# Optimization experiments

Measured on AMD Instinct MI355X. Metric: run time of the kernel, lower is better.

The kernel has to match this reference:

```python
import jax, jax.numpy as jnp
import numpy as np
import math

D_MODEL = 96
D_STATE = 16
D_CONV = 3
EXPAND = 2
D_INNER = EXPAND * D_MODEL          # 192
DT_RANK = math.ceil(D_MODEL / 16)   # 6
B_SZ, H_SZ, W_SZ = 2, 56, 56


def setup_inputs() -> dict:
    key = jax.random.key(0)
    ks = jax.random.split(key, 10)
    x = jax.random.normal(ks[0], (B_SZ, H_SZ, W_SZ, D_MODEL), jnp.float32)
    W_in = jax.random.normal(ks[1], (D_MODEL, 2 * D_INNER), jnp.float32) * 0.02
    conv_w = jax.random.normal(ks[2], (D_CONV, D_CONV, 1, D_INNER), jnp.float32) * 0.1
    conv_b = jax.random.normal(ks[3], (D_INNER,), jnp.float32) * 0.02
    W_xproj = jax.random.normal(ks[4], (D_INNER, DT_RANK + 2 * D_STATE), jnp.float32) * 0.02
    dt_std = DT_RANK ** -0.5
    W_dt = jax.random.uniform(ks[5], (DT_RANK, D_INNER), jnp.float32, -dt_std, dt_std)
    # dt_proj bias init: inverse-softplus of dt ~ LogUniform(dt_min, dt_max)
    dt_min, dt_max = 1e-3, 1e-1
    dt = jnp.exp(jax.random.uniform(ks[6], (D_INNER,), jnp.float32)
                 * (math.log(dt_max) - math.log(dt_min)) + math.log(dt_min))
    dt = jnp.clip(dt, 1e-4, None)
    b_dt = dt + jnp.log(-jnp.expm1(-dt))
    # A_log initialized to broadcast arange(1..d_state) (as in the source, no log taken)
    A_log = jnp.tile(jnp.arange(1, D_STATE + 1, dtype=jnp.float32)[None, :], (D_INNER, 1))
    D_skip = jnp.ones((D_INNER,), jnp.float32)
    W_out = jax.random.normal(ks[7], (D_INNER, D_MODEL), jnp.float32) * 0.02
    return {"x": x, "W_in": W_in, "conv_w": conv_w, "conv_b": conv_b,
            "W_xproj": W_xproj, "W_dt": W_dt, "b_dt": b_dt,
            "A_log": A_log, "D_skip": D_skip, "W_out": W_out}


def _selective_scan(xs, dt, A, Bm, Cm, D_skip):
    """Canonical Mamba selective scan.
    xs, dt: (G, L, C); Bm, Cm: (G, L, N); A: (C, N); D_skip: (C,).
    h_l = exp(dt_l * A) * h_{l-1} + dt_l * B_l * x_l ;  y_l = <h_l, C_l> + D * x_l
    """
    dA = jnp.exp(dt[..., None] * A)                              # (G,L,C,N)
    dBx = dt[..., None] * Bm[:, :, None, :] * xs[..., None]      # (G,L,C,N)

    def step(h, inp):
        dA_l, dBx_l, C_l = inp                                   # (G,C,N),(G,C,N),(G,N)
        h = dA_l * h + dBx_l
        y = jnp.einsum('gcn,gn->gc', h, C_l)
        return h, y

    G, L, C = xs.shape
    h0 = jnp.zeros((G, C, D_STATE), xs.dtype)
    _, ys = jax.lax.scan(step, h0, (jnp.moveaxis(dA, 1, 0),
                                    jnp.moveaxis(dBx, 1, 0),
                                    jnp.moveaxis(Cm, 1, 0)))
    ys = jnp.moveaxis(ys, 0, 1)                                  # (G,L,C)
    return ys + D_skip * xs


def reference(x, W_in, conv_w, conv_b, W_xproj, W_dt, b_dt, A_log, D_skip, W_out):
    B, H, W, _ = x.shape  # H == W required (source sums transposed scans directly)
    xz = x @ W_in                                                # (B,H,W,2*d_inner)
    xm, z = jnp.split(xz, 2, axis=-1)
    pad = (D_CONV - 1) // 2
    xm = jax.lax.conv_general_dilated(
        xm, conv_w, (1, 1), [(pad, pad), (pad, pad)],
        dimension_numbers=('NHWC', 'HWIO', 'NHWC'),
        feature_group_count=D_INNER) + conv_b                    # depthwise conv
    # 4 scan directions
    xt = jnp.swapaxes(xm, 1, 2)
    xs4 = jnp.stack([xm, jnp.flip(xm, 2), xt, jnp.flip(xt, 1)], 0)  # (4,B,H,W,C)
    G, L = 4 * B, H * W
    xs = xs4.reshape(G, L, D_INNER)
    x_dbl = xs @ W_xproj                                          # (G,L,dt_rank+2N)
    dtr, Bm, Cm = jnp.split(x_dbl, [DT_RANK, DT_RANK + D_STATE], axis=-1)
    dt = jax.nn.softplus(dtr @ W_dt + b_dt)                       # (G,L,d_inner)
    A = -jnp.exp(A_log)                                           # (d_inner, N)
    ys = _selective_scan(xs, dt, A, Bm, Cm, D_skip)               # (G,L,d_inner)
    y = ys.reshape(4, B, H, W, D_INNER).sum(0)                    # sum 4 directions
    y = jax.nn.silu(z) * y
    return y @ W_out                                              # (B,H,W,d_model)
```

## Files before the change

### kernel.cpp

```cpp
#include <hip/hip_runtime.h>
#include <math.h>

#define NPIX 6272
#define LVAL 3136
#define CIN 192
#define NST 16
#define HW 56

__device__ __forceinline__ float softplusf(float v) {
    return (v > 20.0f) ? v : log1pf(expf(v));
}

__device__ __forceinline__ void dir_geom(int d, int b, int& si, int& sj, int& off) {
    if (d == 0)      { si = HW;  sj = 1;   off = b * LVAL; }
    else if (d == 1) { si = HW;  sj = -1;  off = b * LVAL + (HW - 1); }
    else if (d == 2) { si = 1;   sj = HW;  off = b * LVAL; }
    else             { si = -1;  sj = HW;  off = b * LVAL + (HW - 1); }
}

__global__ __launch_bounds__(384) void k_inproj(
    const float* __restrict__ x, const float* __restrict__ W_in,
    float* __restrict__ xm, float* __restrict__ z)
{
    __shared__ __align__(16) float xs[96][20];
    const int p0 = blockIdx.x * 16;
    const int t = threadIdx.x;
    for (int e = t; e < 16 * 96; e += 384) {
        int p = e / 96, kk = e % 96;
        xs[kk][p] = x[p0 * 96 + e];
    }
    __syncthreads();
    float acc[16];
#pragma unroll
    for (int p = 0; p < 16; ++p) acc[p] = 0.f;
    for (int k = 0; k < 96; ++k) {
        float w = W_in[k * 384 + t];
        float4 x0 = *(const float4*)&xs[k][0];
        float4 x1 = *(const float4*)&xs[k][4];
        float4 x2 = *(const float4*)&xs[k][8];
        float4 x3 = *(const float4*)&xs[k][12];
        acc[0]  = fmaf(x0.x, w, acc[0]);  acc[1]  = fmaf(x0.y, w, acc[1]);
        acc[2]  = fmaf(x0.z, w, acc[2]);  acc[3]  = fmaf(x0.w, w, acc[3]);
        acc[4]  = fmaf(x1.x, w, acc[4]);  acc[5]  = fmaf(x1.y, w, acc[5]);
        acc[6]  = fmaf(x1.z, w, acc[6]);  acc[7]  = fmaf(x1.w, w, acc[7]);
        acc[8]  = fmaf(x2.x, w, acc[8]);  acc[9]  = fmaf(x2.y, w, acc[9]);
        acc[10] = fmaf(x2.z, w, acc[10]); acc[11] = fmaf(x2.w, w, acc[11]);
        acc[12] = fmaf(x3.x, w, acc[12]); acc[13] = fmaf(x3.y, w, acc[13]);
        acc[14] = fmaf(x3.z, w, acc[14]); acc[15] = fmaf(x3.w, w, acc[15]);
    }
#pragma unroll
    for (int p = 0; p < 16; ++p) {
        int pix = p0 + p;
        if (t < 192) xm[pix * CIN + t] = acc[p];
        else         z[pix * CIN + (t - 192)] = acc[p];
    }
}

__global__ __launch_bounds__(256) void k_conv(
    const float* __restrict__ xm, const float* __restrict__ cw,
    const float* __restrict__ cb, float* __restrict__ xcv)
{
    int e = blockIdx.x * 256 + threadIdx.x;
    if (e >= NPIX * CIN) return;
    int c = e % CIN;
    int pix = e / CIN;
    int w = pix % HW;
    int rest = pix / HW;
    int h = rest % HW;
    int b = rest / HW;
    float acc = cb[c];
#pragma unroll
    for (int ky = 0; ky < 3; ++ky) {
        int hh = h + ky - 1;
        if (hh < 0 || hh >= HW) continue;
#pragma unroll
        for (int kx = 0; kx < 3; ++kx) {
            int ww = w + kx - 1;
            if (ww < 0 || ww >= HW) continue;
            acc = fmaf(xm[((b * HW + hh) * HW + ww) * CIN + c],
                       cw[(ky * 3 + kx) * CIN + c], acc);
        }
    }
    xcv[e] = acc;
}

__global__ __launch_bounds__(256) void k_xproj_dt(
    const float* __restrict__ xcv, const float* __restrict__ W_xproj,
    const float* __restrict__ W_dt, const float* __restrict__ b_dt,
    float* __restrict__ Bp, float* __restrict__ Cp, float* __restrict__ dtp)
{
    __shared__ __align__(16) float xs[192][28];
    __shared__ float dtr_lds[24][8];
    const int p0 = blockIdx.x * 24;
    const int t = threadIdx.x;
    for (int e = t; e < 24 * 192; e += 256) {
        int p = e / 192, kk = e % 192;
        int pix = p0 + p;
        xs[kk][p] = (pix < NPIX) ? xcv[pix * CIN + kk] : 0.f;
    }
    __syncthreads();
    const int j  = t % 40;
    const int pq = t / 40;
    if (pq < 6) {
        const int jc = (j < 38) ? j : 37;
        float a0 = 0.f, a1 = 0.f, a2 = 0.f, a3 = 0.f;
        for (int k = 0; k < 192; ++k) {
            float w = W_xproj[k * 38 + jc];
            float4 xv = *(const float4*)&xs[k][pq * 4];
            a0 = fmaf(xv.x, w, a0); a1 = fmaf(xv.y, w, a1);
            a2 = fmaf(xv.z, w, a2); a3 = fmaf(xv.w, w, a3);
        }
        if (j < 38) {
            float r[4] = {a0, a1, a2, a3};
#pragma unroll
            for (int q = 0; q < 4; ++q) {
                int p = pq * 4 + q;
                int pix = p0 + p;
                if (j < 6) dtr_lds[p][j] = r[q];
                if (pix < NPIX) {
                    if (j < 6)       ;
                    else if (j < 22) Bp[pix * NST + (j - 6)] = r[q];
                    else             Cp[pix * NST + (j - 22)] = r[q];
                }
            }
        }
    }
    __syncthreads();
    for (int e = t; e < 24 * 192; e += 256) {
        int p = e / 192, c = e % 192;
        int pix = p0 + p;
        if (pix >= NPIX) continue;
        float v = b_dt[c];
#pragma unroll
        for (int r = 0; r < 6; ++r)
            v = fmaf(dtr_lds[p][r], W_dt[r * CIN + c], v);
        dtp[pix * CIN + c] = softplusf(v);
    }
}

template<int CHUNK>
__global__ __launch_bounds__(192) void k_scan_p1(
    const float* __restrict__ xcv, const float* __restrict__ dtp,
    const float* __restrict__ Bp, const float* __restrict__ A_log,
    float* __restrict__ Pbuf, float* __restrict__ qbuf)
{
    constexpr int CPR = HW / CHUNK;
    __shared__ __align__(16) float Bs[CHUNK * NST];
    const int g = blockIdx.y;
    const int k = blockIdx.x;
    const int c = threadIdx.x;
    const int d = g >> 1, b = g & 1;
    int si, sj, off;
    dir_geom(d, b, si, sj, off);
    const int base = off + (k / CPR) * si + ((k % CPR) * CHUNK) * sj;

    for (int e = c; e < CHUNK * NST; e += 192) {
        int jj = e >> 4, n = e & 15;
        Bs[e] = Bp[(base + jj * sj) * NST + n];
    }

    const float LOG2E = 1.4426950408889634f;
    float a2[NST];
    {
        const float4* Ar = (const float4*)(A_log + c * NST);
#pragma unroll
        for (int q = 0; q < 4; ++q) {
            float4 v = Ar[q];
            a2[q*4+0] = -expf(v.x) * LOG2E;
            a2[q*4+1] = -expf(v.y) * LOG2E;
            a2[q*4+2] = -expf(v.z) * LOG2E;
            a2[q*4+3] = -expf(v.w) * LOG2E;
        }
    }
    __syncthreads();

    float h[NST], P[NST];
#pragma unroll
    for (int n = 0; n < NST; ++n) { h[n] = 0.f; P[n] = 1.f; }

    float dt_v = dtp[base * CIN + c];
    float x_v  = xcv[base * CIN + c];
    for (int jj = 0; jj < CHUNK; ++jj) {
        float dt_c = dt_v, x_c = x_v;
        int jn = (jj + 1 < CHUNK) ? jj + 1 : jj;
        int pixn = base + jn * sj;
        dt_v = dtp[pixn * CIN + c];
        x_v  = xcv[pixn * CIN + c];
        float dtx = dt_c * x_c;
        float Bv[NST];
        {
            const float4* Brow = (const float4*)(Bs + jj * NST);
#pragma unroll
            for (int q = 0; q < 4; ++q) {
                float4 t = Brow[q];
                Bv[q*4+0]=t.x; Bv[q*4+1]=t.y; Bv[q*4+2]=t.z; Bv[q*4+3]=t.w;
            }
        }
#pragma unroll
        for (int n = 0; n < NST; ++n) {
            float dA = exp2f(dt_c * a2[n]);
            h[n] = fmaf(dA, h[n], dtx * Bv[n]);
            P[n] *= dA;
        }
    }
    float4* Pd = (float4*)(Pbuf + ((size_t)(k * 8 + g) * CIN + c) * NST);
    float4* qd = (float4*)(qbuf + ((size_t)(k * 8 + g) * CIN + c) * NST);
#pragma unroll
    for (int q = 0; q < 4; ++q) {
        Pd[q] = make_float4(P[q*4], P[q*4+1], P[q*4+2], P[q*4+3]);
        qd[q] = make_float4(h[q*4], h[q*4+1], h[q*4+2], h[q*4+3]);
    }
}

__global__ __launch_bounds__(256) void k_scan_fix(
    const float* __restrict__ Pbuf, float* __restrict__ qbuf, int nch)
{
    const int g = blockIdx.y;
    const int lo = blockIdx.x * 256 + threadIdx.x;
    const size_t stride = (size_t)8 * CIN * NST;
    size_t idx  = (size_t)g * CIN * NST + lo;
    size_t pidx = idx;
    float Pr[8], qr[8];
#pragma unroll
    for (int i = 0; i < 8; ++i) { Pr[i] = Pbuf[pidx]; qr[i] = qbuf[pidx]; pidx += stride; }
    float h = 0.f;
    for (int k = 0; k < nch; k += 8) {
        float Pn[8], qn[8];
        if (k + 8 < nch) {
#pragma unroll
            for (int i = 0; i < 8; ++i) {
                Pn[i] = Pbuf[pidx + (size_t)i * stride];
                qn[i] = qbuf[pidx + (size_t)i * stride];
            }
        } else {
#pragma unroll
            for (int i = 0; i < 8; ++i) { Pn[i] = 0.f; qn[i] = 0.f; }
        }
#pragma unroll
        for (int i = 0; i < 8; ++i) {
            qbuf[idx] = h;
            h = fmaf(Pr[i], h, qr[i]);
            idx += stride;
        }
#pragma unroll
        for (int i = 0; i < 8; ++i) { Pr[i] = Pn[i]; qr[i] = qn[i]; }
        pidx += (size_t)8 * stride;
    }
}

template<int CHUNK>
__global__ __launch_bounds__(192) void k_scan_p2(
    const float* __restrict__ xcv, const float* __restrict__ dtp,
    const float* __restrict__ Bp, const float* __restrict__ Cp,
    const float* __restrict__ A_log, const float* __restrict__ D_skip,
    const float* __restrict__ qbuf, float* __restrict__ Y4)
{
    constexpr int CPR = HW / CHUNK;
    __shared__ __align__(16) float Bs[CHUNK * NST];
    __shared__ __align__(16) float Cs[CHUNK * NST];
    const int g = blockIdx.y;
    const int k = blockIdx.x;
    const int c = threadIdx.x;
    const int d = g >> 1, b = g & 1;
    int si, sj, off;
    dir_geom(d, b, si, sj, off);
    const int base = off + (k / CPR) * si + ((k % CPR) * CHUNK) * sj;

    for (int e = c; e < CHUNK * NST; e += 192) {
        int jj = e >> 4, n = e & 15;
        int pa = (base + jj * sj) * NST + n;
        Bs[e] = Bp[pa];
        Cs[e] = Cp[pa];
    }

    const float LOG2E = 1.4426950408889634f;
    float a2[NST];
    {
        const float4* Ar = (const float4*)(A_log + c * NST);
#pragma unroll
        for (int q = 0; q < 4; ++q) {
            float4 v = Ar[q];
            a2[q*4+0] = -expf(v.x) * LOG2E;
            a2[q*4+1] = -expf(v.y) * LOG2E;
            a2[q*4+2] = -expf(v.z) * LOG2E;
            a2[q*4+3] = -expf(v.w) * LOG2E;
        }
    }
    const float Dc = D_skip[c];

    float h[NST];
    {
        const float4* qd = (const float4*)(qbuf + ((size_t)(k * 8 + g) * CIN + c) * NST);
#pragma unroll
        for (int q = 0; q < 4; ++q) {
            float4 v = qd[q];
            h[q*4+0]=v.x; h[q*4+1]=v.y; h[q*4+2]=v.z; h[q*4+3]=v.w;
        }
    }
    __syncthreads();

    float* yo = Y4 + ((size_t)d * NPIX + (size_t)b * LVAL + (size_t)k * CHUNK) * CIN;

    float dt_v = dtp[base * CIN + c];
    float x_v  = xcv[base * CIN + c];
    for (int jj = 0; jj < CHUNK; ++jj) {
        float dt_c = dt_v, x_c = x_v;
        int jn = (jj + 1 < CHUNK) ? jj + 1 : jj;
        int pixn = base + jn * sj;
        dt_v = dtp[pixn * CIN + c];
        x_v  = xcv[pixn * CIN + c];
        float dtx = dt_c * x_c;
        float Bv[NST], Cv[NST];
        {
            const float4* Brow = (const float4*)(Bs + jj * NST);
            const float4* Crow = (const float4*)(Cs + jj * NST);
#pragma unroll
            for (int q = 0; q < 4; ++q) {
                float4 t = Brow[q], u = Crow[q];
                Bv[q*4+0]=t.x; Bv[q*4+1]=t.y; Bv[q*4+2]=t.z; Bv[q*4+3]=t.w;
                Cv[q*4+0]=u.x; Cv[q*4+1]=u.y; Cv[q*4+2]=u.z; Cv[q*4+3]=u.w;
            }
        }
        float yc0 = Dc * x_c, yc1 = 0.f;
#pragma unroll
        for (int n = 0; n < NST; n += 2) {
            float dA0 = exp2f(dt_c * a2[n]);
            float dA1 = exp2f(dt_c * a2[n+1]);
            h[n]   = fmaf(dA0, h[n],   dtx * Bv[n]);
            h[n+1] = fmaf(dA1, h[n+1], dtx * Bv[n+1]);
            yc0 = fmaf(h[n],   Cv[n],   yc0);
            yc1 = fmaf(h[n+1], Cv[n+1], yc1);
        }
        yo[jj * CIN + c] = yc0 + yc1;
    }
}

__global__ __launch_bounds__(192) void k_gateout(
    const float* __restrict__ Y4, const float* __restrict__ z,
    const float* __restrict__ W_out, float* __restrict__ out)
{
    __shared__ __align__(16) float xs[192][20];
    const int p0 = blockIdx.x * 16;
    const int t = threadIdx.x;
    const size_t NP = (size_t)NPIX * CIN;
#pragma unroll
    for (int i = 0; i < 16; ++i) {
        size_t idx = (size_t)(p0 + i) * CIN + t;
        float s = Y4[idx] + Y4[idx + NP] + Y4[idx + 2 * NP] + Y4[idx + 3 * NP];
        float zz = z[idx];
        float sig = 1.f / (1.f + expf(-zz));
        xs[t][i] = zz * sig * s;
    }
    __syncthreads();
    const int j  = t % 96;
    const int ph = t / 96;
    float acc[8];
#pragma unroll
    for (int p = 0; p < 8; ++p) acc[p] = 0.f;
    for (int k = 0; k < 192; ++k) {
        float w = W_out[k * 96 + j];
        float4 x0 = *(const float4*)&xs[k][ph * 8];
        float4 x1 = *(const float4*)&xs[k][ph * 8 + 4];
        acc[0] = fmaf(x0.x, w, acc[0]); acc[1] = fmaf(x0.y, w, acc[1]);
        acc[2] = fmaf(x0.z, w, acc[2]); acc[3] = fmaf(x0.w, w, acc[3]);
        acc[4] = fmaf(x1.x, w, acc[4]); acc[5] = fmaf(x1.y, w, acc[5]);
        acc[6] = fmaf(x1.z, w, acc[6]); acc[7] = fmaf(x1.w, w, acc[7]);
    }
#pragma unroll
    for (int p = 0; p < 8; ++p)
        out[(p0 + ph * 8 + p) * 96 + j] = acc[p];
}

template<int CHUNK>
static void launch_scan(const float* xcv, const float* dtp, const float* Bp,
                        const float* Cp, const float* A_log, const float* D_skip,
                        float* Pbuf, float* qbuf, float* Y4, hipStream_t stream)
{
    const int nch = LVAL / CHUNK;
    k_scan_p1<CHUNK><<<dim3(nch, 8), 192, 0, stream>>>(xcv, dtp, Bp, A_log, Pbuf, qbuf);
    k_scan_fix<<<dim3(12, 8), 256, 0, stream>>>(Pbuf, qbuf, nch);
    k_scan_p2<CHUNK><<<dim3(nch, 8), 192, 0, stream>>>(xcv, dtp, Bp, Cp, A_log, D_skip, qbuf, Y4);
}

extern "C" void kernel_launch(void* const* d_in, const int* in_sizes, int n_in,
                              void* d_out, int out_size, void* d_ws, size_t ws_size,
                              hipStream_t stream) {
    const float* x      = (const float*)d_in[0];
    const float* W_in   = (const float*)d_in[1];
    const float* conv_w = (const float*)d_in[2];
    const float* conv_b = (const float*)d_in[3];
    const float* W_xproj= (const float*)d_in[4];
    const float* W_dt   = (const float*)d_in[5];
    const float* b_dt   = (const float*)d_in[6];
    const float* A_log  = (const float*)d_in[7];
    const float* D_skip = (const float*)d_in[8];
    const float* W_out  = (const float*)d_in[9];
    float* out = (float*)d_out;

    float* ws  = (float*)d_ws;
    float* xm  = ws;
    float* z   = xm  + NPIX * CIN;
    float* xcv = z   + NPIX * CIN;
    float* dtp = xcv + NPIX * CIN;
    float* Bp  = dtp + NPIX * CIN;
    float* Cp  = Bp  + NPIX * NST;
    float* Y4  = Cp  + NPIX * NST;
    float* Pbuf= Y4  + (size_t)4 * NPIX * CIN;

    const size_t base_fl = 9834496;
    const size_t ws_fl = ws_size / 4;
    int chunk;
    if (ws_fl >= base_fl + (size_t)2 * 112 * 24576) chunk = 28;
    else                                            chunk = 56;
    float* qbuf = Pbuf + (size_t)(LVAL / chunk) * 8 * CIN * NST;

    k_inproj  <<<NPIX / 16, 384, 0, stream>>>(x, W_in, xm, z);
    k_conv    <<<(NPIX * CIN) / 256, 256, 0, stream>>>(xm, conv_w, conv_b, xcv);
    k_xproj_dt<<<(NPIX + 23) / 24, 256, 0, stream>>>(xcv, W_xproj, W_dt, b_dt, Bp, Cp, dtp);
    if (chunk == 28) launch_scan<28>(xcv, dtp, Bp, Cp, A_log, D_skip, Pbuf, qbuf, Y4, stream);
    else             launch_scan<56>(xcv, dtp, Bp, Cp, A_log, D_skip, Pbuf, qbuf, Y4, stream);
    k_gateout <<<NPIX / 16, 192, 0, stream>>>(Y4, z, W_out, out);
}
```

Before: 230.2 us.

## Split scan state dimension across two half-waves and compute chunk decay analytically

Both scan passes now use 384 threads per block, with each channel's 16 states split across the two halves of a 64-lane wave (8 states each). The output dot product is combined with a cross-half shuffle. In pass 1, the running product of decays is replaced by exp2 of a times the summed dt. This doubles thread-level parallelism and halves per-thread register state to improve latency hiding, at the cost of duplicated dt/x loads and an extra shuffle per step.

Result: faster. 214.0 us (-7.0%).

```diff
diff --git a/kernel.cpp b/kernel.cpp
--- a/kernel.cpp
+++ b/kernel.cpp
@@ -139,7 +139,7 @@
 }
 
 template<int CHUNK>
-__global__ __launch_bounds__(192) void k_scan_p1(
+__global__ __launch_bounds__(384) void k_scan_p1(
     const float* __restrict__ xcv, const float* __restrict__ dtp,
     const float* __restrict__ Bp, const float* __restrict__ A_log,
     float* __restrict__ Pbuf, float* __restrict__ qbuf)
@@ -148,23 +148,28 @@
     __shared__ __align__(16) float Bs[CHUNK * NST];
     const int g = blockIdx.y;
     const int k = blockIdx.x;
-    const int c = threadIdx.x;
+    const int t = threadIdx.x;
+    const int wv = t >> 6;
+    const int lane = t & 63;
+    const int cl = lane & 31, nh = lane >> 5;
+    const int c = wv * 32 + cl;
+    const int n0 = nh * 8;
     const int d = g >> 1, b = g & 1;
     int si, sj, off;
     dir_geom(d, b, si, sj, off);
     const int base = off + (k / CPR) * si + ((k % CPR) * CHUNK) * sj;
 
-    for (int e = c; e < CHUNK * NST; e += 192) {
+    for (int e = t; e < CHUNK * NST; e += 384) {
         int jj = e >> 4, n = e & 15;
         Bs[e] = Bp[(base + jj * sj) * NST + n];
     }
 
     const float LOG2E = 1.4426950408889634f;
-    float a2[NST];
+    float a2[8];
     {
-        const float4* Ar = (const float4*)(A_log + c * NST);
-#pragma unroll
-        for (int q = 0; q < 4; ++q) {
+        const float4* Ar = (const float4*)(A_log + c * NST + n0);
+#pragma unroll
+        for (int q = 0; q < 2; ++q) {
             float4 v = Ar[q];
             a2[q*4+0] = -expf(v.x) * LOG2E;
             a2[q*4+1] = -expf(v.y) * LOG2E;
@@ -174,9 +179,10 @@
     }
     __syncthreads();
 
-    float h[NST], P[NST];
-#pragma unroll
-    for (int n = 0; n < NST; ++n) { h[n] = 0.f; P[n] = 1.f; }
+    float h[8];
+#pragma unroll
+    for (int i = 0; i < 8; ++i) h[i] = 0.f;
+    float Sdt = 0.f;
 
     float dt_v = dtp[base * CIN + c];
     float x_v  = xcv[base * CIN + c];
@@ -187,29 +193,30 @@
         dt_v = dtp[pixn * CIN + c];
         x_v  = xcv[pixn * CIN + c];
         float dtx = dt_c * x_c;
-        float Bv[NST];
+        Sdt += dt_c;
+        float Bv[8];
         {
-            const float4* Brow = (const float4*)(Bs + jj * NST);
-#pragma unroll
-            for (int q = 0; q < 4; ++q) {
-                float4 t = Brow[q];
-                Bv[q*4+0]=t.x; Bv[q*4+1]=t.y; Bv[q*4+2]=t.z; Bv[q*4+3]=t.w;
-            }
-        }
-#pragma unroll
-        for (int n = 0; n < NST; ++n) {
-            float dA = exp2f(dt_c * a2[n]);
-            h[n] = fmaf(dA, h[n], dtx * Bv[n]);
-            P[n] *= dA;
-        }
-    }
-    float4* Pd = (float4*)(Pbuf + ((size_t)(k * 8 + g) * CIN + c) * NST);
-    float4* qd = (float4*)(qbuf + ((size_t)(k * 8 + g) * CIN + c) * NST);
-#pragma unroll
-    for (int q = 0; q < 4; ++q) {
-        Pd[q] = make_float4(P[q*4], P[q*4+1], P[q*4+2], P[q*4+3]);
-        qd[q] = make_float4(h[q*4], h[q*4+1], h[q*4+2], h[q*4+3]);
-    }
+            const float4* Brow = (const float4*)(Bs + jj * NST + n0);
+            float4 t0 = Brow[0], t1 = Brow[1];
+            Bv[0]=t0.x; Bv[1]=t0.y; Bv[2]=t0.z; Bv[3]=t0.w;
+            Bv[4]=t1.x; Bv[5]=t1.y; Bv[6]=t1.z; Bv[7]=t1.w;
+        }
+#pragma unroll
+        for (int i = 0; i < 8; ++i) {
+            float dA = exp2f(dt_c * a2[i]);
+            h[i] = fmaf(dA, h[i], dtx * Bv[i]);
+        }
+    }
+    float P[8];
+#pragma unroll
+    for (int i = 0; i < 8; ++i) P[i] = exp2f(a2[i] * Sdt);
+
+    float4* Pd = (float4*)(Pbuf + ((size_t)(k * 8 + g) * CIN + c) * NST + n0);
+    float4* qd = (float4*)(qbuf + ((size_t)(k * 8 + g) * CIN + c) * NST + n0);
+    Pd[0] = make_float4(P[0], P[1], P[2], P[3]);
+    Pd[1] = make_float4(P[4], P[5], P[6], P[7]);
+    qd[0] = make_float4(h[0], h[1], h[2], h[3]);
+    qd[1] = make_float4(h[4], h[5], h[6], h[7]);
 }
 
 __global__ __launch_bounds__(256) void k_scan_fix(
@@ -249,7 +256,7 @@
 }
 
 template<int CHUNK>
-__global__ __launch_bounds__(192) void k_scan_p2(
+__global__ __launch_bounds__(384) void k_scan_p2(
     const float* __restrict__ xcv, const float* __restrict__ dtp,
     const float* __restrict__ Bp, const float* __restrict__ Cp,
     const float* __restrict__ A_log, const float* __restrict__ D_skip,
@@ -260,13 +267,18 @@
     __shared__ __align__(16) float Cs[CHUNK * NST];
     const int g = blockIdx.y;
     const int k = blockIdx.x;
-    const int c = threadIdx.x;
+    const int t = threadIdx.x;
+    const int wv = t >> 6;
+    const int lane = t & 63;
+    const int cl = lane & 31, nh = lane >> 5;
+    const int c = wv * 32 + cl;
+    const int n0 = nh * 8;
     const int d = g >> 1, b = g & 1;
     int si, sj, off;
     dir_geom(d, b, si, sj, off);
     const int base = off + (k / CPR) * si + ((k % CPR) * CHUNK) * sj;
 
-    for (int e = c; e < CHUNK * NST; e += 192) {
+    for (int e = t; e < CHUNK * NST; e += 384) {
         int jj = e >> 4, n = e & 15;
         int pa = (base + jj * sj) * NST + n;
         Bs[e] = Bp[pa];
@@ -274,11 +286,11 @@
     }
 
     const float LOG2E = 1.4426950408889634f;
-    float a2[NST];
+    float a2[8];
     {
-        const float4* Ar = (const float4*)(A_log + c * NST);
-#pragma unroll
-        for (int q = 0; q < 4; ++q) {
+        const float4* Ar = (const float4*)(A_log + c * NST + n0);
+#pragma unroll
+        for (int q = 0; q < 2; ++q) {
             float4 v = Ar[q];
             a2[q*4+0] = -expf(v.x) * LOG2E;
             a2[q*4+1] = -expf(v.y) * LOG2E;
@@ -288,14 +300,12 @@
     }
     const float Dc = D_skip[c];
 
-    float h[NST];
+    float h[8];
     {
-        const float4* qd = (const float4*)(qbuf + ((size_t)(k * 8 + g) * CIN + c) * NST);
-#pragma unroll
-        for (int q = 0; q < 4; ++q) {
-            float4 v = qd[q];
-            h[q*4+0]=v.x; h[q*4+1]=v.y; h[q*4+2]=v.z; h[q*4+3]=v.w;
-        }
+        const float4* qd = (const float4*)(qbuf + ((size_t)(k * 8 + g) * CIN + c) * NST + n0);
+        float4 v0 = qd[0], v1 = qd[1];
+        h[0]=v0.x; h[1]=v0.y; h[2]=v0.z; h[3]=v0.w;
+        h[4]=v1.x; h[5]=v1.y; h[6]=v1.z; h[7]=v1.w;
     }
     __syncthreads();
 
@@ -310,28 +320,31 @@
         dt_v = dtp[pixn * CIN + c];
         x_v  = xcv[pixn * CIN + c];
         float dtx = dt_c * x_c;
-        float Bv[NST], Cv[NST];
+        float Bv[8], Cv[8];
         {
-            const float4* Brow = (const float4*)(Bs + jj * NST);
-            const float4* Crow = (const float4*)(Cs + jj * NST);
-#pragma unroll
-            for (int q = 0; q < 4; ++q) {
-                float4 t = Brow[q], u = Crow[q];
-                Bv[q*4+0]=t.x; Bv[q*4+1]=t.y; Bv[q*4+2]=t.z; Bv[q*4+3]=t.w;
-                Cv[q*4+0]=u.x; Cv[q*4+1]=u.y; Cv[q*4+2]=u.z; Cv[q*4+3]=u.w;
-            }
-        }
-        float yc0 = Dc * x_c, yc1 = 0.f;
-#pragma unroll
-        for (int n = 0; n < NST; n += 2) {
-            float dA0 = exp2f(dt_c * a2[n]);
-            float dA1 = exp2f(dt_c * a2[n+1]);
-            h[n]   = fmaf(dA0, h[n],   dtx * Bv[n]);
-            h[n+1] = fmaf(dA1, h[n+1], dtx * Bv[n+1]);
-            yc0 = fmaf(h[n],   Cv[n],   yc0);
-            yc1 = fmaf(h[n+1], Cv[n+1], yc1);
-        }
-        yo[jj * CIN + c] = yc0 + yc1;
+            const float4* Brow = (const float4*)(Bs + jj * NST + n0);
+            const float4* Crow = (const float4*)(Cs + jj * NST + n0);
+            float4 t0 = Brow[0], t1 = Brow[1];
+            float4 u0 = Crow[0], u1 = Crow[1];
+            Bv[0]=t0.x; Bv[1]=t0.y; Bv[2]=t0.z; Bv[3]=t0.w;
+            Bv[4]=t1.x; Bv[5]=t1.y; Bv[6]=t1.z; Bv[7]=t1.w;
+            Cv[0]=u0.x; Cv[1]=u0.y; Cv[2]=u0.z; Cv[3]=u0.w;
+            Cv[4]=u1.x; Cv[5]=u1.y; Cv[6]=u1.z; Cv[7]=u1.w;
+        }
+        float yc0 = 0.f, yc1 = 0.f;
+#pragma unroll
+        for (int i = 0; i < 8; i += 2) {
+            float dA0 = exp2f(dt_c * a2[i]);
+            float dA1 = exp2f(dt_c * a2[i+1]);
+            h[i]   = fmaf(dA0, h[i],   dtx * Bv[i]);
+            h[i+1] = fmaf(dA1, h[i+1], dtx * Bv[i+1]);
+            yc0 = fmaf(h[i],   Cv[i],   yc0);
+            yc1 = fmaf(h[i+1], Cv[i+1], yc1);
+        }
+        float yc = yc0 + yc1;
+        yc += __shfl_xor(yc, 32, 64);
+        if (nh == 0)
+            yo[jj * CIN + c] = fmaf(Dc, x_c, yc);
     }
 }
 
@@ -377,9 +390,9 @@
                         float* Pbuf, float* qbuf, float* Y4, hipStream_t stream)
 {
     const int nch = LVAL / CHUNK;
-    k_scan_p1<CHUNK><<<dim3(nch, 8), 192, 0, stream>>>(xcv, dtp, Bp, A_log, Pbuf, qbuf);
+    k_scan_p1<CHUNK><<<dim3(nch, 8), 384, 0, stream>>>(xcv, dtp, Bp, A_log, Pbuf, qbuf);
     k_scan_fix<<<dim3(12, 8), 256, 0, stream>>>(Pbuf, qbuf, nch);
-    k_scan_p2<CHUNK><<<dim3(nch, 8), 192, 0, stream>>>(xcv, dtp, Bp, Cp, A_log, D_skip, qbuf, Y4);
+    k_scan_p2<CHUNK><<<dim3(nch, 8), 384, 0, stream>>>(xcv, dtp, Bp, Cp, A_log, D_skip, qbuf, Y4);
 }
 
 extern "C" void kernel_launch(void* const* d_in, const int* in_sizes, int n_in,
```
